# Kernel optimization log

Measured on AMD Instinct MI355X. Metric: run time of the kernel, lower is better.

The kernel has to match this reference:

```python
import jax, jax.numpy as jnp
import numpy as np

B, L1, C = 1, 8192, 2048
H, D = 16, 128
L2, LI = 512, 257
P, LA, LF = 2, 512, 64
EPS = 1e-6

def _rms(x, g):
    # RMSNorm in fp32 as in WanRMSNorm
    x = x.astype(jnp.float32)
    return x * jax.lax.rsqrt(jnp.mean(x * x, axis=-1, keepdims=True) + EPS) * g

def _attn(q, k, v, mask=None):
    # q: [b,Lq,h,d], k/v: [b,Lk,h,d], mask broadcastable to [b,h,Lq,Lk]
    scale = 1.0 / np.sqrt(q.shape[-1])
    s = jnp.einsum('bqhd,bkhd->bhqk', q, k) * scale
    if mask is not None:
        s = jnp.where(mask, s, jnp.float32(-1e9))
    p = jax.nn.softmax(s, axis=-1)
    return jnp.einsum('bhqk,bkhd->bqhd', p, v)

def setup_inputs() -> dict:
    key = jax.random.key(0)
    ks = jax.random.split(key, 40)
    nrm = lambda i, shape, s=1.0: jax.random.normal(ks[i], shape, jnp.float32) * s
    inp = {}
    inp['x'] = nrm(0, (B, L1, C))
    inp['context_text'] = nrm(1, (B, L2, C))
    inp['context_img'] = nrm(2, (B, LI, C))
    inp['context_audio'] = nrm(3, (P, B, LA, C))
    inp['context_face'] = nrm(4, (P, B, LF, C))
    inp['context_lens'] = jax.random.randint(ks[5], (B,), L2 // 2, L2 + 1, jnp.int32)
    inp['temporal_mask'] = jnp.ones((B, LA), dtype=bool)
    inp['face_mask'] = jax.random.uniform(ks[6], (P, B, L1, 1), jnp.float32)
    wnames = ['Wq', 'Wk', 'Wv', 'Wo', 'Wki', 'Wvi', 'Wka', 'Wva', 'Wkf', 'Wvf']
    for j, nm in enumerate(wnames):
        inp[nm] = nrm(7 + j, (C, C), 0.02)
        inp['b' + nm[1:]] = jnp.zeros((C,), jnp.float32)
    for nm in ['gq', 'gk', 'gki', 'gka', 'gkf']:
        inp[nm] = jnp.ones((C,), jnp.float32)
    return inp

def reference(x, context_text, context_img, context_audio, context_face, context_lens, temporal_mask, face_mask, Wq, bq, Wk, bk, Wv, bv, Wo, bo, Wki, bki, Wvi, bvi, Wka, bka, Wva, bva, Wkf, bkf, Wvf, bvf, gq, gk, gki, gka, gkf):
    b, l1, c = x.shape
    h, d = H, D
    q = _rms(x @ Wq + bq, gq).reshape(b, l1, h, d)
    # text cross-attention with k_lens masking
    k = _rms(context_text @ Wk + bk, gk).reshape(b, -1, h, d)
    v = (context_text @ Wv + bv).reshape(b, -1, h, d)
    kmask = (jnp.arange(k.shape[1])[None, :] < context_lens[:, None])[:, None, None, :]
    x_txt = _attn(q, k, v, kmask)
    # image cross-attention (unmasked)
    ki = _rms(context_img @ Wki + bki, gki).reshape(b, -1, h, d)
    vi = (context_img @ Wvi + bvi).reshape(b, -1, h, d)
    x_img = _attn(q, ki, vi)
    # per-person face+audio concat attention, face always visible, audio follows temporal_mask
    def person(ca, cf, fm):
        ka = _rms(ca @ Wka + bka, gka).reshape(b, -1, h, d)
        va = (ca @ Wva + bva).reshape(b, -1, h, d)
        kf = _rms(cf @ Wkf + bkf, gkf).reshape(b, -1, h, d)
        vf = (cf @ Wvf + bvf).reshape(b, -1, h, d)
        kc = jnp.concatenate([kf, ka], axis=1)
        vc = jnp.concatenate([vf, va], axis=1)
        m = jnp.concatenate([jnp.ones((b, kf.shape[1]), bool), temporal_mask], axis=-1)[:, None, None, :]
        ax = _attn(q, kc, vc, m)
        return ax.reshape(b, l1, c) * fm  # use_token_mask=True
    af = jax.vmap(person)(context_audio, context_face, face_mask).sum(axis=0)
    out = (x_txt.reshape(b, l1, c) + x_img.reshape(b, l1, c) + af) @ Wo + bo
    return out
```

## Files before the change

kernel.cpp:

```cpp
#include <hip/hip_runtime.h>
#include <hip/hip_bf16.h>
#include <cstdint>
#include <cstddef>


typedef __bf16 bf16_t;
typedef __bf16 bf16x8 __attribute__((ext_vector_type(8)));
typedef __bf16 bf16x4 __attribute__((ext_vector_type(4)));
typedef float  floatx4 __attribute__((ext_vector_type(4)));

__device__ __forceinline__ floatx4 mfma16(bf16x8 a, bf16x8 b, floatx4 c) {
  return __builtin_amdgcn_mfma_f32_16x16x32_bf16(a, b, c, 0, 0, 0);
}

__device__ __forceinline__ float quadsum(float v) {
  v += __shfl_xor(v, 1, 64);
  v += __shfl_xor(v, 2, 64);
  v += __shfl_xor(v, 4, 64);
  v += __shfl_xor(v, 8, 64);
  return v;
}

struct TPairs { const float* src[10]; bf16_t* dst[10]; };

__global__ __launch_bounds__(256) void k_transpose_cast(TPairs p) {
  __shared__ float tile[32][33];
  const float* W  = p.src[blockIdx.z];
  bf16_t*      WT = p.dst[blockIdx.z];
  int tx = threadIdx.x, ty = threadIdx.y;
  int x  = blockIdx.x * 32 + tx;
  int yb = blockIdx.y * 32;
#pragma unroll
  for (int r = 0; r < 4; ++r)
    tile[ty + r * 8][tx] = W[(size_t)(yb + ty + r * 8) * 2048 + x];
  __syncthreads();
  int x2  = yb + tx;
  int y2b = blockIdx.x * 32;
#pragma unroll
  for (int r = 0; r < 4; ++r)
    WT[(size_t)(y2b + ty + r * 8) * 2048 + x2] = (bf16_t)tile[tx][ty + r * 8];
}

struct CvtBatch { const float* src[6]; bf16_t* dst[6]; int n4[6]; };

__global__ __launch_bounds__(256) void k_cvt_multi(CvtBatch b) {
  int pidx = blockIdx.y;
  const float4* in4 = (const float4*)b.src[pidx];
  bf16x4* out4 = (bf16x4*)b.dst[pidx];
  int n4 = b.n4[pidx];
  for (int i = blockIdx.x * blockDim.x + threadIdx.x; i < n4;
       i += gridDim.x * blockDim.x) {
    float4 f = in4[i];
    bf16x4 v;
    v[0] = (bf16_t)f.x; v[1] = (bf16_t)f.y; v[2] = (bf16_t)f.z; v[3] = (bf16_t)f.w;
    out4[i] = v;
  }
}

template <int MODE>
__device__ __forceinline__ void gemm_core(const bf16_t* __restrict__ A,
                                          const bf16_t* __restrict__ BT,
                                          const float* __restrict__ bias,
                                          void* __restrict__ Cout, int M,
                                          int m0, int n0) {
  __shared__ bf16_t As[128 * 40];
  __shared__ bf16_t Bs[128 * 40];
  int tid = threadIdx.x;
  int l = tid & 63, w = tid >> 6;
  int lo = l & 15, hi = l >> 4;
  int wm = (w & 1) * 64, wn = (w >> 1) * 64;
  floatx4 acc[4][4];
#pragma unroll
  for (int i = 0; i < 4; ++i)
#pragma unroll
    for (int j = 0; j < 4; ++j) acc[i][j] = (floatx4){0.f, 0.f, 0.f, 0.f};

  for (int k0 = 0; k0 < 2048; k0 += 32) {
    __syncthreads();
#pragma unroll
    for (int i = 0; i < 2; ++i) {
      int g = tid + i * 256;
      int row = g >> 2, kc = (g & 3) * 8;
      *(bf16x8*)(As + row * 40 + kc) =
          *(const bf16x8*)(A + (size_t)(m0 + row) * 2048 + k0 + kc);
      *(bf16x8*)(Bs + row * 40 + kc) =
          *(const bf16x8*)(BT + (size_t)(n0 + row) * 2048 + k0 + kc);
    }
    __syncthreads();
    bf16x8 af[4], bfr[4];
#pragma unroll
    for (int mt = 0; mt < 4; ++mt)
      af[mt] = *(const bf16x8*)(As + (wm + mt * 16 + lo) * 40 + hi * 8);
#pragma unroll
    for (int nt = 0; nt < 4; ++nt)
      bfr[nt] = *(const bf16x8*)(Bs + (wn + nt * 16 + lo) * 40 + hi * 8);
#pragma unroll
    for (int mt = 0; mt < 4; ++mt)
#pragma unroll
      for (int nt = 0; nt < 4; ++nt)
        acc[mt][nt] = mfma16(af[mt], bfr[nt], acc[mt][nt]);
  }

  float bv[4];
#pragma unroll
  for (int nt = 0; nt < 4; ++nt) bv[nt] = bias[n0 + wn + nt * 16 + lo];

  if constexpr (MODE == 2) {
#pragma unroll
    for (int mt = 0; mt < 4; ++mt) {
      int grow0 = m0 + wm + mt * 16 + hi * 4;
#pragma unroll
      for (int nt = 0; nt < 4; ++nt) {
        int gcol = n0 + wn + nt * 16 + lo;
        bf16_t* cp = (bf16_t*)Cout + (size_t)gcol * 2048 + grow0;
        if (grow0 + 3 < M) {
          bf16x4 vv;
#pragma unroll
          for (int r = 0; r < 4; ++r) vv[r] = (bf16_t)(acc[mt][nt][r] + bv[nt]);
          *(bf16x4*)cp = vv;
        } else {
#pragma unroll
          for (int r = 0; r < 4; ++r)
            if (grow0 + r < M) cp[r] = (bf16_t)(acc[mt][nt][r] + bv[nt]);
        }
      }
    }
  } else {
#pragma unroll
    for (int mt = 0; mt < 4; ++mt) {
#pragma unroll
      for (int r = 0; r < 4; ++r) {
        int grow = m0 + wm + mt * 16 + hi * 4 + r;
        if (grow < M) {
#pragma unroll
          for (int nt = 0; nt < 4; ++nt) {
            int gcol = n0 + wn + nt * 16 + lo;
            float v = acc[mt][nt][r] + bv[nt];
            if constexpr (MODE == 1)
              ((float*)Cout)[(size_t)grow * 2048 + gcol] = v;
            else
              ((bf16_t*)Cout)[(size_t)grow * 2048 + gcol] = (bf16_t)v;
          }
        }
      }
    }
  }
}

template <int MODE>
__global__ __launch_bounds__(256) void k_gemm(const bf16_t* __restrict__ A,
                                              const bf16_t* __restrict__ BT,
                                              const float* __restrict__ bias,
                                              void* __restrict__ Cout, int M) {
  gemm_core<MODE>(A, BT, bias, Cout, M, blockIdx.y * 128, blockIdx.x * 128);
}

struct GemmDesc {
  const bf16_t* A; const bf16_t* BT; const float* bias;
  void* C; int M; int trans;
};
struct GemmBatch { GemmDesc d[12]; };

__global__ __launch_bounds__(256) void k_gemm_batch(GemmBatch b) {
  GemmDesc d = b.d[blockIdx.z];
  int m0 = blockIdx.y * 128;
  if (m0 >= d.M) return;
  if (d.trans)
    gemm_core<2>(d.A, d.BT, d.bias, d.C, d.M, m0, blockIdx.x * 128);
  else
    gemm_core<0>(d.A, d.BT, d.bias, d.C, d.M, m0, blockIdx.x * 128);
}

__device__ __forceinline__ void rms_row(bf16_t* y, const float* g, float extra) {
  int tid = threadIdx.x;
  bf16x8 v = *(bf16x8*)(y + tid * 8);
  float s = 0.f;
#pragma unroll
  for (int j = 0; j < 8; ++j) { float f = (float)v[j]; s += f * f; }
#pragma unroll
  for (int d = 1; d < 64; d <<= 1) s += __shfl_xor(s, d, 64);
  __shared__ float red[4];
  if ((tid & 63) == 0) red[tid >> 6] = s;
  __syncthreads();
  float tot = red[0] + red[1] + red[2] + red[3];
  float sc = rsqrtf(tot * (1.0f / 2048.0f) + 1e-6f) * extra;
#pragma unroll
  for (int j = 0; j < 8; ++j)
    v[j] = (bf16_t)((float)v[j] * sc * g[tid * 8 + j]);
  *(bf16x8*)(y + tid * 8) = v;
}

__global__ __launch_bounds__(256) void k_rms_q(bf16_t* __restrict__ Y,
                                               const float* __restrict__ g,
                                               float extra) {
  rms_row(Y + (size_t)blockIdx.x * 2048, g, extra);
}

__global__ __launch_bounds__(256) void k_rms_arena(bf16_t* __restrict__ Ka,
                                                   const float* gk, const float* gki,
                                                   const float* gka, const float* gkf) {
  int row = blockIdx.x;
  const float* g = row < 512 ? gk
                 : row < 769 ? gki
                 : row < 833 ? gkf
                 : row < 1345 ? gka
                 : row < 1409 ? gkf : gka;
  rms_row(Ka + (size_t)row * 2048, g, 1.0f);
}

__global__ __launch_bounds__(256, 3) void k_attn(const bf16_t* __restrict__ Q,
                                                 const bf16_t* __restrict__ K,
                                                 const bf16_t* __restrict__ VT,
                                                 const int* __restrict__ lens,
                                                 const float* __restrict__ fmask,
                                                 bf16_t* __restrict__ acc) {
  __shared__ bf16_t Ks[64 * 136];
  __shared__ bf16_t Vs[128 * 72];
  __shared__ bf16_t Ps[4][16 * 40];

  int h = blockIdx.y, qt = blockIdx.x;
  int tid = threadIdx.x, w = tid >> 6, l = tid & 63, lo = l & 15, hi = l >> 4;
  int qbase = qt * 64 + w * 16;

  bf16x8 qf[4];
  const bf16_t* qp = Q + (size_t)(qbase + lo) * 2048 + h * 128;
#pragma unroll
  for (int ks = 0; ks < 4; ++ks)
    qf[ks] = *(const bf16x8*)(qp + ks * 32 + hi * 8);

  floatx4 Ot[8];
#pragma unroll
  for (int nt = 0; nt < 8; ++nt) Ot[nt] = (floatx4){0.f, 0.f, 0.f, 0.f};

  int vl0 = lens[0];
  vl0 = vl0 < 1 ? 1 : (vl0 > 512 ? 512 : vl0);
  const int koff_[4] = {0, 512, 769, 1345};
  const int nk_[4]   = {512, 257, 576, 576};

  int krow = 0, kdc = 0, vrow = 0, vkc = 0;
  {
    krow = tid >> 4; kdc = (tid & 15) * 8;
    vrow = tid >> 3; vkc = (tid & 7) * 8;
  }

  for (int src = 0; src < 4; ++src) {
    int koff = koff_[src], nk = nk_[src];
    int vlen = (src == 0) ? vl0 : nk;
    floatx4 Os[8];
#pragma unroll
    for (int nt = 0; nt < 8; ++nt) Os[nt] = (floatx4){0.f, 0.f, 0.f, 0.f};
    float llv[4] = {0.f, 0.f, 0.f, 0.f};

    int ntiles = (vlen + 63) >> 6;

    bf16x8 kp[4], vp[4];
#pragma unroll
    for (int i = 0; i < 4; ++i) {
      kp[i] = *(const bf16x8*)(K + (size_t)(koff + krow + i * 16) * 2048 + h * 128 + kdc);
      vp[i] = *(const bf16x8*)(VT + (size_t)(h * 128 + vrow + i * 32) * 2048 + koff + vkc);
    }

    for (int t = 0; t < ntiles; ++t) {
      __syncthreads();
#pragma unroll
      for (int i = 0; i < 4; ++i) {
        *(bf16x8*)(Ks + (krow + i * 16) * 136 + kdc) = kp[i];
        *(bf16x8*)(Vs + (vrow + i * 32) * 72 + vkc) = vp[i];
      }
      __syncthreads();
      if (t + 1 < ntiles) {
        int kb2 = koff + (t + 1) * 64;
#pragma unroll
        for (int i = 0; i < 4; ++i) {
          kp[i] = *(const bf16x8*)(K + (size_t)(kb2 + krow + i * 16) * 2048 + h * 128 + kdc);
          vp[i] = *(const bf16x8*)(VT + (size_t)(h * 128 + vrow + i * 32) * 2048 + kb2 + vkc);
        }
      }

      floatx4 s[4];
#pragma unroll
      for (int g = 0; g < 4; ++g) s[g] = (floatx4){0.f, 0.f, 0.f, 0.f};
#pragma unroll
      for (int ks = 0; ks < 4; ++ks)
#pragma unroll
        for (int g = 0; g < 4; ++g) {
          bf16x8 kf = *(const bf16x8*)(Ks + (g * 16 + lo) * 136 + ks * 32 + hi * 8);
          s[g] = mfma16(qf[ks], kf, s[g]);
        }

#pragma unroll
      for (int half = 0; half < 2; ++half) {
        int g0 = half * 2, g1 = half * 2 + 1;
        bool va = (t * 64 + g0 * 16 + lo) < vlen;
        bool vb = (t * 64 + g1 * 16 + lo) < vlen;
#pragma unroll
        for (int r = 0; r < 4; ++r) {
          float pa = va ? exp2f(s[g0][r]) : 0.f;
          float pb = vb ? exp2f(s[g1][r]) : 0.f;
          llv[r] += pa + pb;
          Ps[w][(hi * 4 + r) * 40 + lo]      = (bf16_t)pa;
          Ps[w][(hi * 4 + r) * 40 + 16 + lo] = (bf16_t)pb;
        }
        bf16x8 pf = *(const bf16x8*)(Ps[w] + lo * 40 + hi * 8);
        int kb = half * 32 + hi * 8;
#pragma unroll
        for (int nt = 0; nt < 8; ++nt) {
          bf16x8 bv = *(const bf16x8*)(Vs + (nt * 16 + lo) * 72 + kb);
          Os[nt] = mfma16(pf, bv, Os[nt]);
        }
      }
    }

    float fw[4];
#pragma unroll
    for (int r = 0; r < 4; ++r) {
      float ll = quadsum(llv[r]);
      int grow = qbase + hi * 4 + r;
      float f = (src >= 2) ? fmask[(src - 2) * 8192 + grow] : 1.0f;
      fw[r] = f / ll;
    }
    floatx4 fv; fv[0] = fw[0]; fv[1] = fw[1]; fv[2] = fw[2]; fv[3] = fw[3];
#pragma unroll
    for (int nt = 0; nt < 8; ++nt) Ot[nt] += Os[nt] * fv;
  }

#pragma unroll
  for (int nt = 0; nt < 8; ++nt)
#pragma unroll
    for (int r = 0; r < 4; ++r) {
      int grow = qbase + hi * 4 + r;
      acc[(size_t)grow * 2048 + h * 128 + nt * 16 + lo] = (bf16_t)Ot[nt][r];
    }
}

extern "C" void kernel_launch(void* const* d_in, const int* in_sizes, int n_in,
                              void* d_out, int out_size, void* d_ws, size_t ws_size,
                              hipStream_t stream) {
  const float* x     = (const float*)d_in[0];
  const float* ctext = (const float*)d_in[1];
  const float* cimg  = (const float*)d_in[2];
  const float* caud  = (const float*)d_in[3];
  const float* cface = (const float*)d_in[4];
  const int*   lens  = (const int*)d_in[5];
  const float* fmask = (const float*)d_in[7];
  const float* Wf[10]; const float* Bf[10];
  for (int j = 0; j < 10; ++j) {
    Wf[j] = (const float*)d_in[8 + 2 * j];
    Bf[j] = (const float*)d_in[9 + 2 * j];
  }
  const float* gq  = (const float*)d_in[28];
  const float* gk  = (const float*)d_in[29];
  const float* gki = (const float*)d_in[30];
  const float* gka = (const float*)d_in[31];
  const float* gkf = (const float*)d_in[32];
  float* out = (float*)d_out;

  char* p = (char*)d_ws;
  auto alloc = [&](size_t bytes) {
    char* r = p; p += (bytes + 255) & ~(size_t)255; return r;
  };
  const size_t WSZ = (size_t)2048 * 2048 * 2;
  bf16_t* WT  = (bf16_t*)alloc(10 * WSZ);
  bf16_t* xbf = (bf16_t*)alloc((size_t)8192 * 2048 * 2);
  bf16_t* tbf = (bf16_t*)alloc((size_t)512 * 2048 * 2);
  bf16_t* ibf = (bf16_t*)alloc((size_t)512 * 2048 * 2);
  bf16_t* abf = (bf16_t*)alloc((size_t)1024 * 2048 * 2);
  bf16_t* fbf = (bf16_t*)alloc((size_t)256 * 2048 * 2);
  bf16_t* qb  = (bf16_t*)alloc((size_t)8192 * 2048 * 2);
  bf16_t* Ka  = (bf16_t*)alloc((size_t)2048 * 2048 * 2);
  bf16_t* VT  = (bf16_t*)alloc((size_t)2048 * 2048 * 2);
  bf16_t* accb= (bf16_t*)alloc((size_t)8192 * 2048 * 2);

  TPairs tp;
  for (int j = 0; j < 10; ++j) { tp.src[j] = Wf[j]; tp.dst[j] = WT + (size_t)j * 2048 * 2048; }
  k_transpose_cast<<<dim3(64, 64, 10), dim3(32, 8), 0, stream>>>(tp);

  CvtBatch cb;
  cb.src[0] = x;     cb.dst[0] = xbf; cb.n4[0] = 8192 * 2048 / 4;
  cb.src[1] = ctext; cb.dst[1] = tbf; cb.n4[1] = 512 * 2048 / 4;
  cb.src[2] = cimg;  cb.dst[2] = ibf; cb.n4[2] = 257 * 2048 / 4;
  cb.src[3] = caud;  cb.dst[3] = abf; cb.n4[3] = 1024 * 2048 / 4;
  cb.src[4] = cface; cb.dst[4] = fbf; cb.n4[4] = 64 * 2048 / 4;
  cb.src[5] = cface + (size_t)64 * 2048; cb.dst[5] = fbf + (size_t)128 * 2048;
  cb.n4[5] = 64 * 2048 / 4;
  k_cvt_multi<<<dim3(1024, 6), 256, 0, stream>>>(cb);

  k_gemm<0><<<dim3(16, 64), 256, 0, stream>>>(xbf, WT + 0 * (size_t)2048 * 2048,
                                              Bf[0], (void*)qb, 8192);
  GemmBatch gb;
  auto W_ = [&](int i) { return WT + (size_t)i * 2048 * 2048; };
  bf16_t* f1 = fbf + (size_t)128 * 2048;
  bf16_t* a1 = abf + (size_t)512 * 2048;
  gb.d[0]  = {tbf, W_(1), Bf[1], Ka,                        512, 0};
  gb.d[1]  = {tbf, W_(2), Bf[2], VT + 0,                    512, 1};
  gb.d[2]  = {ibf, W_(4), Bf[4], Ka + (size_t)512 * 2048,   257, 0};
  gb.d[3]  = {ibf, W_(5), Bf[5], VT + 512,                  257, 1};
  gb.d[4]  = {fbf, W_(8), Bf[8], Ka + (size_t)769 * 2048,    64, 0};
  gb.d[5]  = {fbf, W_(9), Bf[9], VT + 769,                   64, 1};
  gb.d[6]  = {abf, W_(6), Bf[6], Ka + (size_t)833 * 2048,   512, 0};
  gb.d[7]  = {abf, W_(7), Bf[7], VT + 833,                  512, 1};
  gb.d[8]  = {f1,  W_(8), Bf[8], Ka + (size_t)1345 * 2048,   64, 0};
  gb.d[9]  = {f1,  W_(9), Bf[9], VT + 1345,                  64, 1};
  gb.d[10] = {a1,  W_(6), Bf[6], Ka + (size_t)1409 * 2048,  512, 0};
  gb.d[11] = {a1,  W_(7), Bf[7], VT + 1409,                 512, 1};
  k_gemm_batch<<<dim3(16, 4, 12), 256, 0, stream>>>(gb);

  k_rms_q<<<8192, 256, 0, stream>>>(qb, gq, 0.08838834764831845f * 1.44269504088896340736f);
  k_rms_arena<<<1921, 256, 0, stream>>>(Ka, gk, gki, gka, gkf);

  k_attn<<<dim3(128, 16), 256, 0, stream>>>(qb, Ka, VT, lens, fmask, accb);

  k_gemm<1><<<dim3(16, 64), 256, 0, stream>>>(
      accb, WT + (size_t)3 * 2048 * 2048, Bf[3], (void*)out, 8192);
}
```

Measured before the change: 907.3 us.

## Use async global-to-LDS loads in GEMM and double query rows per attention wave

```diff
diff --git a/kernel.cpp b/kernel.cpp
--- a/kernel.cpp
+++ b/kernel.cpp
@@ -19,6 +19,12 @@
   v += __shfl_xor(v, 4, 64);
   v += __shfl_xor(v, 8, 64);
   return v;
+}
+
+__device__ __forceinline__ void async16(const bf16_t* g, bf16_t* l) {
+  __builtin_amdgcn_global_load_lds(
+      (const __attribute__((address_space(1))) unsigned int*)g,
+      (__attribute__((address_space(3))) unsigned int*)l, 16, 0, 0);
 }
 
 struct TPairs { const float* src[10]; bf16_t* dst[10]; };
@@ -57,14 +63,13 @@
   }
 }
 
-template <int MODE>
 __device__ __forceinline__ void gemm_core(const bf16_t* __restrict__ A,
                                           const bf16_t* __restrict__ BT,
                                           const float* __restrict__ bias,
                                           void* __restrict__ Cout, int M,
-                                          int m0, int n0) {
-  __shared__ bf16_t As[128 * 40];
-  __shared__ bf16_t Bs[128 * 40];
+                                          int m0, int n0, int mode) {
+  __shared__ bf16_t As[128 * 32];
+  __shared__ bf16_t Bs[128 * 32];
   int tid = threadIdx.x;
   int l = tid & 63, w = tid >> 6;
   int lo = l & 15, hi = l >> 4;
@@ -75,25 +80,25 @@
 #pragma unroll
     for (int j = 0; j < 4; ++j) acc[i][j] = (floatx4){0.f, 0.f, 0.f, 0.f};
 
+  const bf16_t* Ag = A  + (size_t)(m0 + w * 32 + (l >> 2)) * 2048 + (l & 3) * 8;
+  const bf16_t* Bg = BT + (size_t)(n0 + w * 32 + (l >> 2)) * 2048 + (l & 3) * 8;
+  bf16_t* Al = As + (w * 32) * 32;
+  bf16_t* Bl = Bs + (w * 32) * 32;
+
   for (int k0 = 0; k0 < 2048; k0 += 32) {
     __syncthreads();
-#pragma unroll
-    for (int i = 0; i < 2; ++i) {
-      int g = tid + i * 256;
-      int row = g >> 2, kc = (g & 3) * 8;
-      *(bf16x8*)(As + row * 40 + kc) =
-          *(const bf16x8*)(A + (size_t)(m0 + row) * 2048 + k0 + kc);
-      *(bf16x8*)(Bs + row * 40 + kc) =
-          *(const bf16x8*)(BT + (size_t)(n0 + row) * 2048 + k0 + kc);
-    }
+    async16(Ag + k0, Al);
+    async16(Ag + k0 + 16 * 2048, Al + 16 * 32);
+    async16(Bg + k0, Bl);
+    async16(Bg + k0 + 16 * 2048, Bl + 16 * 32);
     __syncthreads();
     bf16x8 af[4], bfr[4];
 #pragma unroll
     for (int mt = 0; mt < 4; ++mt)
-      af[mt] = *(const bf16x8*)(As + (wm + mt * 16 + lo) * 40 + hi * 8);
+      af[mt] = *(const bf16x8*)(As + (wm + mt * 16 + lo) * 32 + hi * 8);
 #pragma unroll
     for (int nt = 0; nt < 4; ++nt)
-      bfr[nt] = *(const bf16x8*)(Bs + (wn + nt * 16 + lo) * 40 + hi * 8);
+      bfr[nt] = *(const bf16x8*)(Bs + (wn + nt * 16 + lo) * 32 + hi * 8);
 #pragma unroll
     for (int mt = 0; mt < 4; ++mt)
 #pragma unroll
@@ -105,7 +110,7 @@
 #pragma unroll
   for (int nt = 0; nt < 4; ++nt) bv[nt] = bias[n0 + wn + nt * 16 + lo];
 
-  if constexpr (MODE == 2) {
+  if (mode == 2) {
 #pragma unroll
     for (int mt = 0; mt < 4; ++mt) {
       int grow0 = m0 + wm + mt * 16 + hi * 4;
@@ -136,7 +141,7 @@
           for (int nt = 0; nt < 4; ++nt) {
             int gcol = n0 + wn + nt * 16 + lo;
             float v = acc[mt][nt][r] + bv[nt];
-            if constexpr (MODE == 1)
+            if (mode == 1)
               ((float*)Cout)[(size_t)grow * 2048 + gcol] = v;
             else
               ((bf16_t*)Cout)[(size_t)grow * 2048 + gcol] = (bf16_t)v;
@@ -152,7 +157,7 @@
                                               const bf16_t* __restrict__ BT,
                                               const float* __restrict__ bias,
                                               void* __restrict__ Cout, int M) {
-  gemm_core<MODE>(A, BT, bias, Cout, M, blockIdx.y * 128, blockIdx.x * 128);
+  gemm_core(A, BT, bias, Cout, M, blockIdx.y * 128, blockIdx.x * 128, MODE);
 }
 
 struct GemmDesc {
@@ -165,10 +170,8 @@
   GemmDesc d = b.d[blockIdx.z];
   int m0 = blockIdx.y * 128;
   if (m0 >= d.M) return;
-  if (d.trans)
-    gemm_core<2>(d.A, d.BT, d.bias, d.C, d.M, m0, blockIdx.x * 128);
-  else
-    gemm_core<0>(d.A, d.BT, d.bias, d.C, d.M, m0, blockIdx.x * 128);
+  gemm_core(d.A, d.BT, d.bias, d.C, d.M, m0, blockIdx.x * 128,
+            d.trans ? 2 : 0);
 }
 
 __device__ __forceinline__ void rms_row(bf16_t* y, const float* g, float extra) {
@@ -208,7 +211,7 @@
   rms_row(Ka + (size_t)row * 2048, g, 1.0f);
 }
 
-__global__ __launch_bounds__(256, 3) void k_attn(const bf16_t* __restrict__ Q,
+__global__ __launch_bounds__(256, 2) void k_attn(const bf16_t* __restrict__ Q,
                                                  const bf16_t* __restrict__ K,
                                                  const bf16_t* __restrict__ VT,
                                                  const int* __restrict__ lens,
@@ -216,40 +219,44 @@
                                                  bf16_t* __restrict__ acc) {
   __shared__ bf16_t Ks[64 * 136];
   __shared__ bf16_t Vs[128 * 72];
-  __shared__ bf16_t Ps[4][16 * 40];
+  __shared__ bf16_t Ps[4][32 * 40];
 
   int h = blockIdx.y, qt = blockIdx.x;
   int tid = threadIdx.x, w = tid >> 6, l = tid & 63, lo = l & 15, hi = l >> 4;
-  int qbase = qt * 64 + w * 16;
-
-  bf16x8 qf[4];
-  const bf16_t* qp = Q + (size_t)(qbase + lo) * 2048 + h * 128;
-#pragma unroll
-  for (int ks = 0; ks < 4; ++ks)
-    qf[ks] = *(const bf16x8*)(qp + ks * 32 + hi * 8);
-
-  floatx4 Ot[8];
-#pragma unroll
-  for (int nt = 0; nt < 8; ++nt) Ot[nt] = (floatx4){0.f, 0.f, 0.f, 0.f};
+  int qbase = qt * 128 + w * 32;
+
+  bf16x8 qf[2][4];
+#pragma unroll
+  for (int rg = 0; rg < 2; ++rg) {
+    const bf16_t* qp = Q + (size_t)(qbase + rg * 16 + lo) * 2048 + h * 128;
+#pragma unroll
+    for (int ks = 0; ks < 4; ++ks)
+      qf[rg][ks] = *(const bf16x8*)(qp + ks * 32 + hi * 8);
+  }
+
+  floatx4 Ot[2][8];
+#pragma unroll
+  for (int rg = 0; rg < 2; ++rg)
+#pragma unroll
+    for (int nt = 0; nt < 8; ++nt) Ot[rg][nt] = (floatx4){0.f, 0.f, 0.f, 0.f};
 
   int vl0 = lens[0];
   vl0 = vl0 < 1 ? 1 : (vl0 > 512 ? 512 : vl0);
   const int koff_[4] = {0, 512, 769, 1345};
   const int nk_[4]   = {512, 257, 576, 576};
 
-  int krow = 0, kdc = 0, vrow = 0, vkc = 0;
-  {
-    krow = tid >> 4; kdc = (tid & 15) * 8;
-    vrow = tid >> 3; vkc = (tid & 7) * 8;
-  }
+  int krow = tid >> 4, kdc = (tid & 15) * 8;
+  int vrow = tid >> 3, vkc = (tid & 7) * 8;
 
   for (int src = 0; src < 4; ++src) {
-    int koff = koff_[src], nk = nk_[src];
-    int vlen = (src == 0) ? vl0 : nk;
-    floatx4 Os[8];
-#pragma unroll
-    for (int nt = 0; nt < 8; ++nt) Os[nt] = (floatx4){0.f, 0.f, 0.f, 0.f};
-    float llv[4] = {0.f, 0.f, 0.f, 0.f};
+    int koff = koff_[src];
+    int vlen = (src == 0) ? vl0 : nk_[src];
+    floatx4 Os[2][8];
+#pragma unroll
+    for (int rg = 0; rg < 2; ++rg)
+#pragma unroll
+      for (int nt = 0; nt < 8; ++nt) Os[rg][nt] = (floatx4){0.f, 0.f, 0.f, 0.f};
+    float llv[2][4] = {{0.f, 0.f, 0.f, 0.f}, {0.f, 0.f, 0.f, 0.f}};
 
     int ntiles = (vlen + 63) >> 6;
 
@@ -277,60 +284,71 @@
         }
       }
 
-      floatx4 s[4];
-#pragma unroll
-      for (int g = 0; g < 4; ++g) s[g] = (floatx4){0.f, 0.f, 0.f, 0.f};
-#pragma unroll
-      for (int ks = 0; ks < 4; ++ks)
-#pragma unroll
-        for (int g = 0; g < 4; ++g) {
-          bf16x8 kf = *(const bf16x8*)(Ks + (g * 16 + lo) * 136 + ks * 32 + hi * 8);
-          s[g] = mfma16(qf[ks], kf, s[g]);
+#pragma unroll
+      for (int hf = 0; hf < 2; ++hf) {
+        floatx4 s[2][2];
+#pragma unroll
+        for (int rg = 0; rg < 2; ++rg)
+#pragma unroll
+          for (int g = 0; g < 2; ++g) s[rg][g] = (floatx4){0.f, 0.f, 0.f, 0.f};
+#pragma unroll
+        for (int ks = 0; ks < 4; ++ks) {
+          bf16x8 kf0 = *(const bf16x8*)(Ks + ((hf * 2 + 0) * 16 + lo) * 136 + ks * 32 + hi * 8);
+          bf16x8 kf1 = *(const bf16x8*)(Ks + ((hf * 2 + 1) * 16 + lo) * 136 + ks * 32 + hi * 8);
+          s[0][0] = mfma16(qf[0][ks], kf0, s[0][0]);
+          s[1][0] = mfma16(qf[1][ks], kf0, s[1][0]);
+          s[0][1] = mfma16(qf[0][ks], kf1, s[0][1]);
+          s[1][1] = mfma16(qf[1][ks], kf1, s[1][1]);
         }
-
-#pragma unroll
-      for (int half = 0; half < 2; ++half) {
-        int g0 = half * 2, g1 = half * 2 + 1;
-        bool va = (t * 64 + g0 * 16 + lo) < vlen;
-        bool vb = (t * 64 + g1 * 16 + lo) < vlen;
-#pragma unroll
-        for (int r = 0; r < 4; ++r) {
-          float pa = va ? exp2f(s[g0][r]) : 0.f;
-          float pb = vb ? exp2f(s[g1][r]) : 0.f;
-          llv[r] += pa + pb;
-          Ps[w][(hi * 4 + r) * 40 + lo]      = (bf16_t)pa;
-          Ps[w][(hi * 4 + r) * 40 + 16 + lo] = (bf16_t)pb;
-        }
-        bf16x8 pf = *(const bf16x8*)(Ps[w] + lo * 40 + hi * 8);
-        int kb = half * 32 + hi * 8;
+        bool va = (t * 64 + (hf * 2 + 0) * 16 + lo) < vlen;
+        bool vb = (t * 64 + (hf * 2 + 1) * 16 + lo) < vlen;
+#pragma unroll
+        for (int rg = 0; rg < 2; ++rg)
+#pragma unroll
+          for (int r = 0; r < 4; ++r) {
+            float pa = va ? exp2f(s[rg][0][r]) : 0.f;
+            float pb = vb ? exp2f(s[rg][1][r]) : 0.f;
+            llv[rg][r] += pa + pb;
+            Ps[w][(rg * 16 + hi * 4 + r) * 40 + lo]      = (bf16_t)pa;
+            Ps[w][(rg * 16 + hi * 4 + r) * 40 + 16 + lo] = (bf16_t)pb;
+          }
+        bf16x8 pf0 = *(const bf16x8*)(Ps[w] + (lo) * 40 + hi * 8);
+        bf16x8 pf1 = *(const bf16x8*)(Ps[w] + (16 + lo) * 40 + hi * 8);
+        int kb = hf * 32 + hi * 8;
 #pragma unroll
         for (int nt = 0; nt < 8; ++nt) {
           bf16x8 bv = *(const bf16x8*)(Vs + (nt * 16 + lo) * 72 + kb);
-          Os[nt] = mfma16(pf, bv, Os[nt]);
+          Os[0][nt] = mfma16(pf0, bv, Os[0][nt]);
+          Os[1][nt] = mfma16(pf1, bv, Os[1][nt]);
         }
       }
     }
 
-    float fw[4];
-#pragma unroll
-    for (int r = 0; r < 4; ++r) {
-      float ll = quadsum(llv[r]);
-      int grow = qbase + hi * 4 + r;
-      float f = (src >= 2) ? fmask[(src - 2) * 8192 + grow] : 1.0f;
-      fw[r] = f / ll;
+#pragma unroll
+    for (int rg = 0; rg < 2; ++rg) {
+      float fw[4];
+#pragma unroll
+      for (int r = 0; r < 4; ++r) {
+        float ll = quadsum(llv[rg][r]);
+        int grow = qbase + rg * 16 + hi * 4 + r;
+        float f = (src >= 2) ? fmask[(src - 2) * 8192 + grow] : 1.0f;
+        fw[r] = f / ll;
+      }
+      floatx4 fv; fv[0] = fw[0]; fv[1] = fw[1]; fv[2] = fw[2]; fv[3] = fw[3];
+#pragma unroll
+      for (int nt = 0; nt < 8; ++nt) Ot[rg][nt] += Os[rg][nt] * fv;
     }
-    floatx4 fv; fv[0] = fw[0]; fv[1] = fw[1]; fv[2] = fw[2]; fv[3] = fw[3];
-#pragma unroll
-    for (int nt = 0; nt < 8; ++nt) Ot[nt] += Os[nt] * fv;
-  }
-
-#pragma unroll
-  for (int nt = 0; nt < 8; ++nt)
-#pragma unroll
-    for (int r = 0; r < 4; ++r) {
-      int grow = qbase + hi * 4 + r;
-      acc[(size_t)grow * 2048 + h * 128 + nt * 16 + lo] = (bf16_t)Ot[nt][r];
-    }
+  }
+
+#pragma unroll
+  for (int rg = 0; rg < 2; ++rg)
+#pragma unroll
+    for (int nt = 0; nt < 8; ++nt)
+#pragma unroll
+      for (int r = 0; r < 4; ++r) {
+        int grow = qbase + rg * 16 + hi * 4 + r;
+        acc[(size_t)grow * 2048 + h * 128 + nt * 16 + lo] = (bf16_t)Ot[rg][nt][r];
+      }
 }
 
 extern "C" void kernel_launch(void* const* d_in, const int* in_sizes, int n_in,
@@ -408,7 +426,7 @@
   k_rms_q<<<8192, 256, 0, stream>>>(qb, gq, 0.08838834764831845f * 1.44269504088896340736f);
   k_rms_arena<<<1921, 256, 0, stream>>>(Ka, gk, gki, gka, gkf);
 
-  k_attn<<<dim3(128, 16), 256, 0, stream>>>(qb, Ka, VT, lens, fmask, accb);
+  k_attn<<<dim3(64, 16), 256, 0, stream>>>(qb, Ka, VT, lens, fmask, accb);
 
   k_gemm<1><<<dim3(16, 64), 256, 0, stream>>>(
       accb, WT + (size_t)3 * 2048 * 2048, Bf[3], (void*)out, 8192);
```

After: 813.4 us. -10.4%, faster.
